# Optimization experiments

Measured on AMD Instinct MI355X. Metric: run time of the kernel, lower is better.

## Reference

```python
import jax, jax.numpy as jnp
import numpy as np
from jax import lax

MAX_C = 16       # MAX_MERGE_NUMS
COND_THRES = 0.2
IOU_THRES = 0.3
CLASS_OFFSET = 1e4  # shift per-class so cross-class BEV IoU == 0 (emulates per-class loop)


def setup_inputs() -> dict:
    key = jax.random.key(0)
    k1, k2, k3, k4, k5 = jax.random.split(key, 5)
    B, N = 4, 4096
    # realistic 3D boxes: centers, positive sizes, heading
    centers = jax.random.normal(k1, (B, N, 3), jnp.float32) * 20.0
    sizes = jax.random.uniform(k2, (B, N, 3), jnp.float32, 0.5, 4.5)
    heading = jax.random.uniform(k3, (B, N, 1), jnp.float32, -np.pi, np.pi)
    boxes = jnp.concatenate([centers, sizes, heading], -1)  # [B,N,7]
    scores = jax.random.uniform(k4, (B, N), jnp.float32)
    labels = jax.random.randint(k5, (B, N), 0, 3, jnp.int32)
    kw = jax.random.split(jax.random.fold_in(key, 1), 2)
    W1 = jax.random.normal(kw[0], (7, 64), jnp.float32) * 0.3
    b1 = jnp.zeros((64,), jnp.float32)
    W2 = jax.random.normal(kw[1], (64, 1), jnp.float32) * 0.3
    b2 = jnp.zeros((1,), jnp.float32)
    return {"boxes": boxes, "scores": scores, "labels": labels,
            "W1": W1, "b1": b1, "W2": W2, "b2": b2}


def _nms_merge_frame(boxes, scores, labels, W1, b1, W2, b2):
    # boxes [N,7], scores [N], labels [N] int32
    N = boxes.shape[0]
    valid = scores > COND_THRES                       # cond_mask
    skey = jnp.where(valid, scores, -jnp.inf)
    order = jnp.argsort(-skey)                        # score descending
    boxes, scores = boxes[order], scores[order]
    labels, valid = labels[order], valid[order]

    # nearest-BEV (axis-aligned) IoU; class offset keeps classes disjoint
    off = labels.astype(boxes.dtype) * CLASS_OFFSET
    cx, cy = boxes[:, 0] + off, boxes[:, 1]
    hx, hy = boxes[:, 3] * 0.5, boxes[:, 4] * 0.5
    x1, x2, y1, y2 = cx - hx, cx + hx, cy - hy, cy + hy
    ix = jnp.clip(jnp.minimum(x2[:, None], x2[None]) - jnp.maximum(x1[:, None], x1[None]), 0.0)
    iy = jnp.clip(jnp.minimum(y2[:, None], y2[None]) - jnp.maximum(y1[:, None], y1[None]), 0.0)
    inter = ix * iy                                   # [N,N]
    area = (x2 - x1) * (y2 - y1)
    iou = inter / jnp.clip(area[:, None] + area[None] - inter, 1e-6)
    overlap = iou > IOU_THRES                         # includes self

    # greedy clustering: highest-score remaining box leads its cluster
    def body(i, st):
        alive, cid = st
        lead = alive[i]
        take = alive & overlap[i] & lead
        cid = jnp.where(take, i, cid)
        return alive & (~take), cid
    alive, cid = lax.fori_loop(0, N, body,
                               (valid, jnp.full((N,), -1, jnp.int32)))
    leader = cid == jnp.arange(N, dtype=jnp.int32)    # cluster representatives

    # rank of each box within its cluster (score order preserved)
    idx = jnp.arange(N)
    same = (cid[None, :] == cid[:, None]) & (cid[:, None] >= 0)
    rank = (same & (idx[None, :] < idx[:, None])).sum(-1)  # [N]

    # scatter up to MAX_C members per cluster (zero-padded buffers)
    dest = jnp.where((cid >= 0) & (rank < MAX_C), cid, N)  # N = dump row
    clusters = jnp.zeros((N + 1, MAX_C, 7), boxes.dtype)
    clusters = clusters.at[dest, jnp.minimum(rank, MAX_C - 1)].set(boxes)[:N]

    # merge network: per-box MLP -> softmax weights over cluster slots
    h = jax.nn.relu(clusters @ W1 + b1)               # [N,MAX_C,64]
    logits = (h @ W2 + b2)[..., 0]                    # [N,MAX_C]
    slot_ok = jnp.any(clusters != 0, -1)
    logits = jnp.where(slot_ok, logits, -1e9)
    w = jax.nn.softmax(logits, -1)
    merged = jnp.einsum('nc,ncd->nd', w, clusters)    # [N,7]

    # masked scatter: non-positive merged sizes fall back to leader sizes
    size = jnp.where(merged[:, 3:6] <= 0, boxes[:, 3:6], merged[:, 3:6])
    out_box = jnp.concatenate([merged[:, :3], size, merged[:, 6:7]], -1)
    info = jnp.concatenate([out_box, scores[:, None],
                            labels.astype(boxes.dtype)[:, None]], -1)  # [N,9]
    info = jnp.where(leader[:, None], info, 0.0)
    return info, leader


def reference(boxes, scores, labels, W1, b1, W2, b2):
    info, leader = jax.vmap(_nms_merge_frame,
                            in_axes=(0, 0, 0, None, None, None, None))(
        boxes, scores, labels, W1, b1, W2, b2)
    return info, leader
```

## Files before the change

kernel.cpp:

```cpp
#include <hip/hip_runtime.h>
#include <stdint.h>

#pragma clang fp contract(off)

#define BF 4
#define NN 4096
#define MAXC 16
#define PL 2048
#define WL 32

typedef unsigned long long u64;
typedef uint32_t u32;

__device__ __forceinline__ u64 shfl64(u64 v, int src) {
  return (u64)__shfl((long long)v, src, 64);
}

__global__ __launch_bounds__(1024) void sort_kernel(
    const float* __restrict__ scores, u64* __restrict__ keyS)
{
  __shared__ u64 keyA[NN];
  __shared__ u64 keyB[NN];
  __shared__ int cnt16[16][65];
  __shared__ int waveTot[16];
  __shared__ int waveBase[16];
  const int f = blockIdx.x, tid = threadIdx.x;
  const int wave = tid >> 6, lane = tid & 63;
  const u64 ltmask = (1ull << lane) - 1ull;

  for (int s = 0; s < 4; s++) {
    int idx = tid + 1024 * s;
    float sc = scores[f * NN + idx];
    bool valid = sc > 0.2f;
    u32 bits = __float_as_uint(sc);
    u32 m = bits ^ ((bits >> 31) ? 0xFFFFFFFFu : 0x80000000u);
    u32 hi = valid ? ~m : 0xFFFFFFFFu;
    keyA[idx] = ((u64)hi << 32) | (u32)idx;
  }
  __syncthreads();

  u64* src = keyA;
  u64* dst = keyB;
  for (int pass = 0; pass < 7; pass++) {
    const int shift = 32 + 4 * pass;
    u64 kreg[4]; int dreg[4], rreg[4];
    for (int s = 0; s < 4; s++) {
      const int c = wave * 4 + s;
      u64 k = src[c * 64 + lane];
      int d = (int)((k >> shift) & 15);
      u64 B0 = __ballot((d & 1) != 0);
      u64 B1 = __ballot((d & 2) != 0);
      u64 B2 = __ballot((d & 4) != 0);
      u64 B3 = __ballot((d & 8) != 0);
      u64 M = ((d & 1) ? B0 : ~B0) & ((d & 2) ? B1 : ~B1)
            & ((d & 4) ? B2 : ~B2) & ((d & 8) ? B3 : ~B3);
      rreg[s] = __popcll(M & ltmask);
      int bin = lane & 15;
      u64 Mb = ((bin & 1) ? B0 : ~B0) & ((bin & 2) ? B1 : ~B1)
             & ((bin & 4) ? B2 : ~B2) & ((bin & 8) ? B3 : ~B3);
      if (lane < 16) cnt16[bin][c] = __popcll(Mb);
      kreg[s] = k; dreg[s] = d;
    }
    __syncthreads();
    {
      int v = cnt16[wave][lane];
      int incl = v;
      for (int off2 = 1; off2 < 64; off2 <<= 1) {
        int up = __shfl_up(incl, off2, 64);
        if (lane >= off2) incl += up;
      }
      if (lane == 63) waveTot[wave] = incl;
      __syncthreads();
      if (wave == 0) {
        int tv = (lane < 16) ? waveTot[lane] : 0;
        int ts = tv;
        for (int off2 = 1; off2 < 16; off2 <<= 1) {
          int up = __shfl_up(ts, off2, 64);
          if (lane >= off2) ts += up;
        }
        if (lane < 16) waveBase[lane] = ts - tv;
      }
      __syncthreads();
      cnt16[wave][lane] = waveBase[wave] + incl - v;
    }
    __syncthreads();
    for (int s = 0; s < 4; s++) {
      const int c = wave * 4 + s;
      int pos = cnt16[dreg[s]][c] + rreg[s];
      dst[pos] = kreg[s];
    }
    __syncthreads();
    u64* tmp = src; src = dst; dst = tmp;
  }
  for (int s = 0; s < 4; s++) {
    int p = tid + 1024 * s;
    keyS[f * NN + p] = src[p];
  }
}

__global__ __launch_bounds__(256) void counts_kernel(
    const u64* __restrict__ keyS, const int* __restrict__ labels,
    int* __restrict__ chunkCnt)
{
  const int gs = blockIdx.x * 256 + threadIdx.x;
  const int f = gs >> 12, p = gs & (NN - 1);
  const int lane = threadIdx.x & 63, chunk = p >> 6;
  u64 kv = keyS[gs];
  bool valid = (u32)(kv >> 32) != 0xFFFFFFFFu;
  int g = (int)(kv & 0xFFFFFFFFull);
  int l = valid ? labels[f * NN + g] : 3;
  u64 B0 = __ballot((l & 1) != 0);
  u64 B1 = __ballot((l & 2) != 0);
  if (lane < 3) {
    u64 Mb = ((lane & 1) ? B0 : ~B0) & ((lane & 2) ? B1 : ~B1);
    chunkCnt[(f * 64 + chunk) * 3 + lane] = __popcll(Mb);
  }
}

__global__ __launch_bounds__(64) void scan_kernel(
    const int* __restrict__ chunkCnt, int* __restrict__ chunkOffG,
    int* __restrict__ VbufL)
{
  const int f = blockIdx.x, lane = threadIdx.x;
  for (int ll = 0; ll < 3; ll++) {
    int v = chunkCnt[(f * 64 + lane) * 3 + ll];
    int incl = v;
    for (int off2 = 1; off2 < 64; off2 <<= 1) {
      int up = __shfl_up(incl, off2, 64);
      if (lane >= off2) incl += up;
    }
    chunkOffG[(f * 64 + lane) * 3 + ll] = incl - v;
    if (lane == 63) VbufL[f * 3 + ll] = incl;
  }
}

__global__ __launch_bounds__(256) void gather_kernel(
    const u64* __restrict__ keyS, const float* __restrict__ boxes,
    const float* __restrict__ scores, const int* __restrict__ labels,
    const int* __restrict__ chunkOffG,
    float* __restrict__ sboxes, float* __restrict__ sscore, float* __restrict__ slabel,
    int* __restrict__ lab_slot, int* __restrict__ loc_slot,
    int* __restrict__ pglob,
    float* __restrict__ px1, float* __restrict__ px2, float* __restrict__ py1,
    float* __restrict__ py2, float* __restrict__ parea)
{
  const int gs = blockIdx.x * 256 + threadIdx.x;
  const int f = gs >> 12, p = gs & (NN - 1);
  const int lane = threadIdx.x & 63, chunk = p >> 6;
  const u64 ltmask = (1ull << lane) - 1ull;
  u64 kv = keyS[gs];
  bool valid = (u32)(kv >> 32) != 0xFFFFFFFFu;
  int g = (int)(kv & 0xFFFFFFFFull);
  const float* bp = boxes + (size_t)(f * NN + g) * 7;
  float b0 = bp[0], b1v = bp[1], b2v = bp[2], b3 = bp[3], b4 = bp[4], b5 = bp[5], b6 = bp[6];
  int lab = labels[f * NN + g];
  const int o = f * NN + p;
  float* sb = sboxes + (size_t)o * 7;
  sb[0] = b0; sb[1] = b1v; sb[2] = b2v; sb[3] = b3; sb[4] = b4; sb[5] = b5; sb[6] = b6;
  sscore[o] = scores[f * NN + g];
  slabel[o] = (float)lab;
  int l = valid ? lab : 3;
  u64 B0 = __ballot((l & 1) != 0);
  u64 B1 = __ballot((l & 2) != 0);
  u64 M = ((l & 1) ? B0 : ~B0) & ((l & 2) ? B1 : ~B1);
  int rank = __popcll(M & ltmask);
  if (l < 3) {
    int loc = chunkOffG[(f * 64 + chunk) * 3 + l] + rank;
    int pi = (f * 3 + l) * PL + loc;
    float off = (float)l * 10000.0f;
    float cx = b0 + off, cy = b1v;
    float hx = b3 * 0.5f, hy = b4 * 0.5f;
    float x1 = cx - hx, x2 = cx + hx, y1 = cy - hy, y2 = cy + hy;
    float area = (x2 - x1) * (y2 - y1);
    pglob[pi] = p;
    px1[pi] = x1; px2[pi] = x2; py1[pi] = y1; py2[pi] = y2; parea[pi] = area;
    lab_slot[o] = l; loc_slot[o] = loc;
  } else {
    lab_slot[o] = -1; loc_slot[o] = -1;
  }
}

__global__ __launch_bounds__(256) void mask_kernel(
    const float* __restrict__ px1, const float* __restrict__ px2,
    const float* __restrict__ py1, const float* __restrict__ py2,
    const float* __restrict__ parea, const int* __restrict__ pglob,
    const int* __restrict__ VbufL,
    u64* __restrict__ maskP, u64* __restrict__ maskT)
{
  __shared__ float4 cbox[1024];
  __shared__ float carea[1024];
  const int bx = blockIdx.x;
  const int fl = bx >> 8, rem = bx & 255;
  const int rt = rem >> 1, wt = rem & 1;
  const int r0 = rt * 16;
  const int Vl = VbufL[fl];
  if (r0 >= Vl) return;
  if (wt * 1024 >= Vl) return;
  const int tid = threadIdx.x;
  for (int q = tid; q < 1024; q += 256) {
    int c = fl * PL + wt * 1024 + q;
    cbox[q] = make_float4(px1[c], px2[c], py1[c], py2[c]);
    carea[q] = parea[c];
  }
  __syncthreads();
  const int row = r0 + (tid & 15);
  const int wl = tid >> 4;
  if (row >= Vl) return;
  const int rg = fl * PL + row;
  const float rx1 = px1[rg], rx2 = px2[rg], ry1 = py1[rg], ry2 = py2[rg], ra = parea[rg];
  u64 bits = 0;
  const int qb = wl * 64;
  for (int b = 0; b < 64; b++) {
    float4 cb = cbox[qb + b];
    float ca = carea[qb + b];
    float ix = fminf(rx2, cb.y) - fmaxf(rx1, cb.x);
    ix = fmaxf(ix, 0.0f);
    float iy = fminf(ry2, cb.w) - fmaxf(ry1, cb.z);
    iy = fmaxf(iy, 0.0f);
    float inter = ix * iy;
    float den = fmaxf((ra + ca) - inter, 1e-6f);
    float iou = inter / den;
    bits |= ((u64)(iou > 0.3f)) << b;
  }
  const int cw = wt * 16 + wl;
  const int nc = Vl - cw * 64;
  if (nc <= 0) return;
  if (nc < 64) bits &= (1ull << nc) - 1ull;
  const int f = fl / 3;
  const int p = pglob[fl * PL + row];
  maskP[((size_t)f * NN + p) * WL + cw] = bits;
  maskT[((size_t)fl * WL + cw) * PL + row] = bits;
}

__global__ __launch_bounds__(64) void nms_kernel(
    const u64* __restrict__ maskT, const int* __restrict__ VbufL,
    u64* __restrict__ leadersP)
{
  __shared__ u64 buf[2][PL];
  const int fl = blockIdx.x, lane = threadIdx.x;
  const int Vl = VbufL[fl];
  const int W = (Vl + 63) >> 6;
  const u64* mT = maskT + (size_t)fl * WL * PL;
  u64 alive = 0;
  if (lane < WL) {
    int rb = Vl - 64 * lane;
    alive = (rb >= 64) ? ~0ull : ((rb > 0) ? ((1ull << rb) - 1ull) : 0ull);
  }
  u64 myLead = 0;
  {
    const char* g = (const char*)mT;
    char* l0 = (char*)&buf[0][0];
    for (int it = 0; it < 16; it++)
      __builtin_amdgcn_global_load_lds(
          (const __attribute__((address_space(1))) unsigned int*)(g + (size_t)it * 1024 + (size_t)lane * 16),
          (__attribute__((address_space(3))) unsigned int*)(l0 + (size_t)it * 1024),
          16, 0, 0);
  }
  for (int w = 0; w < W; w++) {
    const int par = w & 1;
    if (w + 1 < W) {
      const char* g = (const char*)(mT + ((size_t)(w + 1)) * PL + (size_t)64 * (w + 1));
      char* l1 = (char*)&buf[1 - par][0];
      for (int it = 0; it < 16; it++)
        __builtin_amdgcn_global_load_lds(
            (const __attribute__((address_space(1))) unsigned int*)(g + (size_t)it * 1024 + (size_t)lane * 16),
            (__attribute__((address_space(3))) unsigned int*)(l1 + (size_t)it * 1024),
            16, 0, 0);
    asm volatile("s_waitcnt vmcnt(16)" ::: "memory");
    } else {
      asm volatile("s_waitcnt vmcnt(0)" ::: "memory");
    }
    u64 D = buf[par][lane];
    u32 alo = (u32)__builtin_amdgcn_readlane((int)(u32)alive, w);
    u32 ahi = (u32)__builtin_amdgcn_readlane((int)(u32)(alive >> 32), w);
    u64 rem = ((u64)ahi << 32) | alo;
    u64 lead = 0;
    while (rem) {
      int b = __builtin_ctzll(rem);
      lead |= 1ull << b;
      u32 dlo = (u32)__builtin_amdgcn_readlane((int)(u32)D, b);
      u32 dhi = (u32)__builtin_amdgcn_readlane((int)(u32)(D >> 32), b);
      rem &= ~(((u64)dhi << 32) | dlo);
    }
    if (lane == w) myLead = lead;
    for (int v = w; v < W; v++) {
      u64 val = buf[par][64 * (v - w) + lane];
      u64 bal = __ballot((val & lead) != 0ull);
      if (lane == v) alive &= ~bal;
    }
  }
  if (lane < WL) leadersP[fl * WL + lane] = myLead;
}

__global__ __launch_bounds__(256) void cid_kernel(
    const u64* __restrict__ maskP, const u64* __restrict__ leadersP,
    const int* __restrict__ lab_slot, const int* __restrict__ loc_slot,
    const int* __restrict__ VbufL, int* __restrict__ cidP)
{
  const int g = blockIdx.x * 4 + (threadIdx.x >> 6);
  const int lane = threadIdx.x & 63;
  const int f = g >> 12, p = g & (NN - 1);
  const int l = lab_slot[f * NN + p];
  if (l < 0) return;
  const int fl = f * 3 + l;
  const int loc = loc_slot[f * NN + p];
  const int Wl = (VbufL[fl] + 63) >> 6;
  u64 L = 0, m = 0;
  if (lane < Wl) {
    L = leadersP[fl * WL + lane];
    m = maskP[((size_t)f * NN + p) * WL + lane];
  }
  const int g6 = loc >> 6, b6 = loc & 63;
  u64 pmask = (lane < g6) ? ~0ull
            : (lane == g6 ? ((b6 == 63) ? ~0ull : ((1ull << (b6 + 1)) - 1ull)) : 0ull);
  u64 v = m & L & pmask;
  u64 bl = __ballot(v != 0ull);
  int cid = -1;
  if (bl != 0ull) {
    int w = __builtin_ctzll(bl);
    u64 vw = shfl64(v, w);
    cid = w * 64 + __builtin_ctzll(vw);
  }
  if (lane == 0) cidP[fl * PL + loc] = cid;
}

__global__ __launch_bounds__(64) void mm_kernel(
    const u64* __restrict__ maskP, const u64* __restrict__ leadersP,
    const int* __restrict__ cidP, const int* __restrict__ lab_slot,
    const int* __restrict__ loc_slot, const int* __restrict__ pglob,
    const int* __restrict__ VbufL,
    const float* __restrict__ sboxes, const float* __restrict__ sscore,
    const float* __restrict__ slabel,
    const float* __restrict__ W1, const float* __restrict__ b1,
    const float* __restrict__ W2, const float* __restrict__ b2,
    float* __restrict__ out)
{
  const int bi = blockIdx.x;
  const int f = bi >> 12, i = bi & (NN - 1);
  const int lane = threadIdx.x;
  const int o = f * NN + i;
  float* info = out + (size_t)o * 9;
  float* lead = out + (size_t)BF * NN * 9 + o;
  const int l = lab_slot[o];
  bool isLead = false;
  int loc = 0, fl = 0;
  if (l >= 0) {
    fl = f * 3 + l;
    loc = loc_slot[o];
    isLead = (leadersP[fl * WL + (loc >> 6)] >> (loc & 63)) & 1ull;
  }
  if (!isLead) {
    if (lane < 9) info[lane] = 0.0f;
    if (lane == 0) *lead = 0.0f;
    return;
  }
  __shared__ int mlist[MAXC];
  __shared__ float mb[MAXC][7];
  __shared__ float lg[MAXC];
  __shared__ float wn[MAXC];
  const u64* mrow = maskP + (size_t)o * WL;
  const int Wl = (VbufL[fl] + 63) >> 6;
  int total = 0;
  for (int w = loc >> 6; w < Wl && total < MAXC; w++) {
    u64 word = mrow[w];
    int pos = w * 64 + lane;
    bool cand = ((word >> lane) & 1ull) && (cidP[fl * PL + pos] == loc);
    u64 mbal = __ballot(cand);
    int r = __popcll(mbal & ((1ull << lane) - 1ull));
    int slot = total + r;
    if (cand && slot < MAXC) mlist[slot] = pglob[fl * PL + pos];
    total += __popcll(mbal);
  }
  const int cnt = min(total, MAXC);
  __syncthreads();
  if (lane < cnt) {
    int j = mlist[lane];
    const float* bp = sboxes + (size_t)(f * NN + j) * 7;
    for (int d = 0; d < 7; d++) mb[lane][d] = bp[d];
  }
  float w1r[7];
  for (int d = 0; d < 7; d++) w1r[d] = W1[d * 64 + lane];
  const float b1c = b1[lane], w2c = W2[lane], b2v = b2[0];
  __syncthreads();
  for (int s = 0; s < cnt; s++) {
    float t = b1c;
    for (int d = 0; d < 7; d++) t += mb[s][d] * w1r[d];
    float h = fmaxf(t, 0.0f);
    float v = h * w2c;
    for (int off2 = 32; off2 > 0; off2 >>= 1) v += __shfl_xor(v, off2, 64);
    if (lane == 0) lg[s] = v + b2v;
  }
  __syncthreads();
  float mx = -1e30f;
  for (int s = 0; s < cnt; s++) mx = fmaxf(mx, lg[s]);
  float den = 0.0f;
  for (int s = 0; s < cnt; s++) den += expf(lg[s] - mx);
  if (lane < cnt) wn[lane] = expf(lg[lane] - mx) / den;
  __syncthreads();
  float val = 0.0f;
  if (lane < 7) {
    float acc = 0.0f;
    for (int s = 0; s < cnt; s++) acc += wn[s] * mb[s][lane];
    val = acc;
    if (lane >= 3 && lane <= 5 && val <= 0.0f) val = sboxes[(size_t)o * 7 + lane];
  } else if (lane == 7) {
    val = sscore[o];
  } else if (lane == 8) {
    val = slabel[o];
  }
  if (lane < 9) info[lane] = val;
  if (lane == 0) *lead = 1.0f;
}

extern "C" void kernel_launch(void* const* d_in, const int* in_sizes, int n_in,
                              void* d_out, int out_size, void* d_ws, size_t ws_size,
                              hipStream_t stream)
{
  const float* boxes  = (const float*)d_in[0];
  const float* scores = (const float*)d_in[1];
  const int*   labels = (const int*)d_in[2];
  const float* W1     = (const float*)d_in[3];
  const float* b1     = (const float*)d_in[4];
  const float* W2     = (const float*)d_in[5];
  const float* b2     = (const float*)d_in[6];
  float* out = (float*)d_out;

  char* ws = (char*)d_ws;
  size_t off = 0;
  auto alloc = [&](size_t bytes) -> void* {
    void* p = ws + off;
    off = (off + bytes + 255) & ~(size_t)255;
    return p;
  };
  u64*   keyS    = (u64*)  alloc((size_t)BF * NN * 8);
  int*   chunkCnt= (int*)  alloc((size_t)BF * 64 * 3 * 4);
  int*   chunkOffG=(int*)  alloc((size_t)BF * 64 * 3 * 4);
  float* sboxes  = (float*)alloc((size_t)BF * NN * 7 * 4);
  float* sscore  = (float*)alloc((size_t)BF * NN * 4);
  float* slabel  = (float*)alloc((size_t)BF * NN * 4);
  int*   lab_slot= (int*)  alloc((size_t)BF * NN * 4);
  int*   loc_slot= (int*)  alloc((size_t)BF * NN * 4);
  int*   pglob   = (int*)  alloc((size_t)BF * 3 * PL * 4);
  float* px1     = (float*)alloc((size_t)BF * 3 * PL * 4);
  float* px2     = (float*)alloc((size_t)BF * 3 * PL * 4);
  float* py1     = (float*)alloc((size_t)BF * 3 * PL * 4);
  float* py2     = (float*)alloc((size_t)BF * 3 * PL * 4);
  float* parea   = (float*)alloc((size_t)BF * 3 * PL * 4);
  int*   VbufL   = (int*)  alloc((size_t)BF * 3 * 4);
  u64*   leadersP= (u64*)  alloc((size_t)BF * 3 * WL * 8);
  int*   cidP    = (int*)  alloc((size_t)BF * 3 * PL * 4);
  u64*   maskP   = (u64*)  alloc((size_t)BF * NN * WL * 8);
  u64*   maskT   = (u64*)  alloc((size_t)BF * 3 * WL * PL * 8);
  (void)  alloc(32768);

  sort_kernel<<<BF, 1024, 0, stream>>>(scores, keyS);
  counts_kernel<<<BF * NN / 256, 256, 0, stream>>>(keyS, labels, chunkCnt);
  scan_kernel<<<BF, 64, 0, stream>>>(chunkCnt, chunkOffG, VbufL);
  gather_kernel<<<BF * NN / 256, 256, 0, stream>>>(keyS, boxes, scores, labels,
                                                   chunkOffG, sboxes, sscore,
                                                   slabel, lab_slot, loc_slot,
                                                   pglob, px1, px2, py1, py2,
                                                   parea);
  mask_kernel<<<BF * 3 * 256, 256, 0, stream>>>(px1, px2, py1, py2, parea,
                                                pglob, VbufL, maskP, maskT);
  nms_kernel<<<BF * 3, 64, 0, stream>>>(maskT, VbufL, leadersP);
  cid_kernel<<<BF * NN / 4, 256, 0, stream>>>(maskP, leadersP, lab_slot,
                                              loc_slot, VbufL, cidP);
  mm_kernel<<<BF * NN, 64, 0, stream>>>(maskP, leadersP, cidP, lab_slot,
                                        loc_slot, pglob, VbufL, sboxes,
                                        sscore, slabel, W1, b1, W2, b2, out);
}
```

Before: 192.1 us.

## Fuse count and scan kernels, trim NMS DMA and unroll suppression ballots

```diff
diff --git a/kernel.cpp b/kernel.cpp
--- a/kernel.cpp
+++ b/kernel.cpp
@@ -14,6 +14,11 @@
 
 __device__ __forceinline__ u64 shfl64(u64 v, int src) {
   return (u64)__shfl((long long)v, src, 64);
+}
+__device__ __forceinline__ u64 readlane64(u64 v, int l) {
+  u32 lo = (u32)__builtin_amdgcn_readlane((int)(u32)v, l);
+  u32 hi = (u32)__builtin_amdgcn_readlane((int)(u32)(v >> 32), l);
+  return ((u64)hi << 32) | lo;
 }
 
 __global__ __launch_bounds__(1024) void sort_kernel(
@@ -98,39 +103,39 @@
   }
 }
 
-__global__ __launch_bounds__(256) void counts_kernel(
+__global__ __launch_bounds__(256) void countscan_kernel(
     const u64* __restrict__ keyS, const int* __restrict__ labels,
-    int* __restrict__ chunkCnt)
-{
-  const int gs = blockIdx.x * 256 + threadIdx.x;
-  const int f = gs >> 12, p = gs & (NN - 1);
-  const int lane = threadIdx.x & 63, chunk = p >> 6;
-  u64 kv = keyS[gs];
-  bool valid = (u32)(kv >> 32) != 0xFFFFFFFFu;
-  int g = (int)(kv & 0xFFFFFFFFull);
-  int l = valid ? labels[f * NN + g] : 3;
-  u64 B0 = __ballot((l & 1) != 0);
-  u64 B1 = __ballot((l & 2) != 0);
-  if (lane < 3) {
-    u64 Mb = ((lane & 1) ? B0 : ~B0) & ((lane & 2) ? B1 : ~B1);
-    chunkCnt[(f * 64 + chunk) * 3 + lane] = __popcll(Mb);
-  }
-}
-
-__global__ __launch_bounds__(64) void scan_kernel(
-    const int* __restrict__ chunkCnt, int* __restrict__ chunkOffG,
-    int* __restrict__ VbufL)
-{
-  const int f = blockIdx.x, lane = threadIdx.x;
-  for (int ll = 0; ll < 3; ll++) {
-    int v = chunkCnt[(f * 64 + lane) * 3 + ll];
-    int incl = v;
-    for (int off2 = 1; off2 < 64; off2 <<= 1) {
-      int up = __shfl_up(incl, off2, 64);
-      if (lane >= off2) incl += up;
-    }
-    chunkOffG[(f * 64 + lane) * 3 + ll] = incl - v;
-    if (lane == 63) VbufL[f * 3 + ll] = incl;
+    int* __restrict__ chunkOffG, int* __restrict__ VbufL)
+{
+  __shared__ int cnt[64][3];
+  const int f = blockIdx.x, tid = threadIdx.x;
+  const int wave = tid >> 6, lane = tid & 63;
+  for (int s = 0; s < 16; s++) {
+    int chunk = wave * 16 + s;
+    int p = chunk * 64 + lane;
+    u64 kv = keyS[f * NN + p];
+    bool valid = (u32)(kv >> 32) != 0xFFFFFFFFu;
+    int g = (int)(kv & 0xFFFFFFFFull);
+    int l = valid ? labels[f * NN + g] : 3;
+    u64 B0 = __ballot((l & 1) != 0);
+    u64 B1 = __ballot((l & 2) != 0);
+    if (lane < 3) {
+      u64 Mb = ((lane & 1) ? B0 : ~B0) & ((lane & 2) ? B1 : ~B1);
+      cnt[chunk][lane] = __popcll(Mb);
+    }
+  }
+  __syncthreads();
+  if (wave == 0) {
+    for (int ll = 0; ll < 3; ll++) {
+      int v = cnt[lane][ll];
+      int incl = v;
+      for (int off2 = 1; off2 < 64; off2 <<= 1) {
+        int up = __shfl_up(incl, off2, 64);
+        if (lane >= off2) incl += up;
+      }
+      chunkOffG[(f * 64 + lane) * 3 + ll] = incl - v;
+      if (lane == 63) VbufL[f * 3 + ll] = incl;
+    }
   }
 }
 
@@ -205,7 +210,9 @@
   __syncthreads();
   const int row = r0 + (tid & 15);
   const int wl = tid >> 4;
-  if (row >= Vl) return;
+  const int cw = wt * 16 + wl;
+  const int nc = Vl - cw * 64;
+  if (row >= Vl || nc <= 0) return;
   const int rg = fl * PL + row;
   const float rx1 = px1[rg], rx2 = px2[rg], ry1 = py1[rg], ry2 = py2[rg], ra = parea[rg];
   u64 bits = 0;
@@ -222,9 +229,6 @@
     float iou = inter / den;
     bits |= ((u64)(iou > 0.3f)) << b;
   }
-  const int cw = wt * 16 + wl;
-  const int nc = Vl - cw * 64;
-  if (nc <= 0) return;
   if (nc < 64) bits &= (1ull << nc) - 1ull;
   const int f = fl / 3;
   const int p = pglob[fl * PL + row];
@@ -232,11 +236,24 @@
   maskT[((size_t)fl * WL + cw) * PL + row] = bits;
 }
 
+__device__ __forceinline__ void dma16(const u64* gbase, u64* lbase, int nch, int lane) {
+  const char* g = (const char*)gbase;
+#pragma unroll
+  for (int it = 0; it < 16; it++) {
+    int itc = (it < nch) ? it : (nch - 1);
+    __builtin_amdgcn_global_load_lds(
+        (const __attribute__((address_space(1))) unsigned int*)(g + (size_t)itc * 1024 + (size_t)lane * 16),
+        (__attribute__((address_space(3))) unsigned int*)((char*)lbase + (size_t)it * 1024),
+        16, 0, 0);
+  }
+}
+
 __global__ __launch_bounds__(64) void nms_kernel(
     const u64* __restrict__ maskT, const int* __restrict__ VbufL,
     u64* __restrict__ leadersP)
 {
-  __shared__ u64 buf[2][PL];
+  __shared__ u64 bufA[PL];
+  __shared__ u64 bufB[PL];
   const int fl = blockIdx.x, lane = threadIdx.x;
   const int Vl = VbufL[fl];
   const int W = (Vl + 63) >> 6;
@@ -247,48 +264,56 @@
     alive = (rb >= 64) ? ~0ull : ((rb > 0) ? ((1ull << rb) - 1ull) : 0ull);
   }
   u64 myLead = 0;
-  {
-    const char* g = (const char*)mT;
-    char* l0 = (char*)&buf[0][0];
-    for (int it = 0; it < 16; it++)
-      __builtin_amdgcn_global_load_lds(
-          (const __attribute__((address_space(1))) unsigned int*)(g + (size_t)it * 1024 + (size_t)lane * 16),
-          (__attribute__((address_space(3))) unsigned int*)(l0 + (size_t)it * 1024),
-          16, 0, 0);
-  }
-  for (int w = 0; w < W; w++) {
-    const int par = w & 1;
-    if (w + 1 < W) {
-      const char* g = (const char*)(mT + ((size_t)(w + 1)) * PL + (size_t)64 * (w + 1));
-      char* l1 = (char*)&buf[1 - par][0];
-      for (int it = 0; it < 16; it++)
-        __builtin_amdgcn_global_load_lds(
-            (const __attribute__((address_space(1))) unsigned int*)(g + (size_t)it * 1024 + (size_t)lane * 16),
-            (__attribute__((address_space(3))) unsigned int*)(l1 + (size_t)it * 1024),
-            16, 0, 0);
-    asm volatile("s_waitcnt vmcnt(16)" ::: "memory");
-    } else {
-      asm volatile("s_waitcnt vmcnt(0)" ::: "memory");
-    }
-    u64 D = buf[par][lane];
-    u32 alo = (u32)__builtin_amdgcn_readlane((int)(u32)alive, w);
-    u32 ahi = (u32)__builtin_amdgcn_readlane((int)(u32)(alive >> 32), w);
-    u64 rem = ((u64)ahi << 32) | alo;
-    u64 lead = 0;
-    while (rem) {
-      int b = __builtin_ctzll(rem);
-      lead |= 1ull << b;
-      u32 dlo = (u32)__builtin_amdgcn_readlane((int)(u32)D, b);
-      u32 dhi = (u32)__builtin_amdgcn_readlane((int)(u32)(D >> 32), b);
-      rem &= ~(((u64)dhi << 32) | dlo);
-    }
-    if (lane == w) myLead = lead;
-    for (int v = w; v < W; v++) {
-      u64 val = buf[par][64 * (v - w) + lane];
-      u64 bal = __ballot((val & lead) != 0ull);
-      if (lane == v) alive &= ~bal;
-    }
-  }
+
+#define NMS_STEP(WV, RB, DB)                                                  \
+  {                                                                           \
+    const int w_ = (WV);                                                      \
+    int s_ = w_ + 1; if (s_ >= W) s_ = W - 1;                                 \
+    int nch_ = (W - s_ + 1) >> 1; if (nch_ < 1) nch_ = 1;                     \
+    dma16(mT + (size_t)s_ * PL + (size_t)64 * s_, DB, nch_, lane);            \
+    asm volatile("s_waitcnt vmcnt(16)" ::: "memory");                         \
+    u64 D_ = RB[lane];                                                        \
+    u64 rem_ = readlane64(alive, w_);                                         \
+    u64 lead_ = 0;                                                            \
+    while (rem_) {                                                            \
+      int b_ = __builtin_ctzll(rem_);                                         \
+      lead_ |= 1ull << b_;                                                    \
+      rem_ &= ~readlane64(D_, b_);                                            \
+    }                                                                         \
+    if (lane == w_) myLead = lead_;                                           \
+    if (lead_) {                                                              \
+      int v_ = w_ + 1;                                                        \
+      for (; v_ + 3 < W; v_ += 4) {                                           \
+        u64 a0 = RB[64 * (v_ - w_) + lane];                                   \
+        u64 a1 = RB[64 * (v_ + 1 - w_) + lane];                               \
+        u64 a2 = RB[64 * (v_ + 2 - w_) + lane];                               \
+        u64 a3 = RB[64 * (v_ + 3 - w_) + lane];                               \
+        u64 b0 = __ballot((a0 & lead_) != 0ull);                              \
+        u64 b1 = __ballot((a1 & lead_) != 0ull);                              \
+        u64 b2 = __ballot((a2 & lead_) != 0ull);                              \
+        u64 b3 = __ballot((a3 & lead_) != 0ull);                              \
+        if (lane == v_)     alive &= ~b0;                                     \
+        if (lane == v_ + 1) alive &= ~b1;                                     \
+        if (lane == v_ + 2) alive &= ~b2;                                     \
+        if (lane == v_ + 3) alive &= ~b3;                                     \
+      }                                                                       \
+      for (; v_ < W; v_++) {                                                  \
+        u64 a0 = RB[64 * (v_ - w_) + lane];                                   \
+        u64 b0 = __ballot((a0 & lead_) != 0ull);                              \
+        if (lane == v_) alive &= ~b0;                                         \
+      }                                                                       \
+    }                                                                         \
+  }
+
+  if (W > 0) {
+    dma16(mT, bufA, (W + 1) >> 1, lane);
+    for (int w = 0; w < W; w += 2) {
+      NMS_STEP(w, bufA, bufB);
+      if (w + 1 < W) NMS_STEP(w + 1, bufB, bufA);
+    }
+  }
+  asm volatile("s_waitcnt vmcnt(0)" ::: "memory");
+#undef NMS_STEP
   if (lane < WL) leadersP[fl * WL + lane] = myLead;
 }
 
@@ -433,7 +458,6 @@
     return p;
   };
   u64*   keyS    = (u64*)  alloc((size_t)BF * NN * 8);
-  int*   chunkCnt= (int*)  alloc((size_t)BF * 64 * 3 * 4);
   int*   chunkOffG=(int*)  alloc((size_t)BF * 64 * 3 * 4);
   float* sboxes  = (float*)alloc((size_t)BF * NN * 7 * 4);
   float* sscore  = (float*)alloc((size_t)BF * NN * 4);
@@ -454,8 +478,7 @@
   (void)  alloc(32768);
 
   sort_kernel<<<BF, 1024, 0, stream>>>(scores, keyS);
-  counts_kernel<<<BF * NN / 256, 256, 0, stream>>>(keyS, labels, chunkCnt);
-  scan_kernel<<<BF, 64, 0, stream>>>(chunkCnt, chunkOffG, VbufL);
+  countscan_kernel<<<BF, 256, 0, stream>>>(keyS, labels, chunkOffG, VbufL);
   gather_kernel<<<BF * NN / 256, 256, 0, stream>>>(keyS, boxes, scores, labels,
                                                    chunkOffG, sboxes, sscore,
                                                    slabel, lab_slot, loc_slot,
```

Result: slower. 200.3 us (+4.3%).
